# Kernel optimization log

Measured on AMD Instinct MI355X. Metric: run time of the kernel, lower is better.

Reference implementation:

```python
import jax, jax.numpy as jnp
import numpy as np
import math

B, S, D, H = 16, 1024, 1024, 16
HD = D // H                      # 64 head dim
MLP_H = int(int(D * 4.0) * 2 / 3)  # 2730 SwiGLU hidden
EPS = 1e-6


def _rmsnorm(h, w):
    # fp32 RMSNorm over last dim
    v = jnp.mean(h * h, axis=-1, keepdims=True)
    return w * (h * jax.lax.rsqrt(v + EPS))


def _rope(x):
    # x: [B, H, S, HD]; standard rotary, half-split convention
    hd = x.shape[-1]
    pos = jnp.arange(x.shape[-2], dtype=jnp.float32)
    inv = 1.0 / (10000.0 ** (jnp.arange(0, hd, 2, dtype=jnp.float32) / hd))
    fr = pos[:, None] * inv[None, :]          # [S, HD/2]
    cos, sin = jnp.cos(fr), jnp.sin(fr)
    x1, x2 = jnp.split(x, 2, axis=-1)
    return jnp.concatenate([x1 * cos - x2 * sin, x1 * sin + x2 * cos], axis=-1)


def setup_inputs() -> dict:
    key = jax.random.key(0)
    ks = jax.random.split(key, 16)
    sc = 0.02
    return {
        "x": jax.random.normal(ks[0], (B, S, D), jnp.float32),
        "c": jax.random.normal(ks[1], (B, D), jnp.float32),
        "w_qkv": jax.random.normal(ks[2], (D, 3 * D), jnp.float32) * sc,
        "b_qkv": jnp.zeros((3 * D,), jnp.float32),
        "w_proj": jax.random.normal(ks[3], (D, D), jnp.float32) * sc,
        "b_proj": jnp.zeros((D,), jnp.float32),
        "w12": jax.random.normal(ks[4], (D, 2 * MLP_H), jnp.float32) * sc,
        "b12": jnp.zeros((2 * MLP_H,), jnp.float32),
        "w3": jax.random.normal(ks[5], (MLP_H, D), jnp.float32) * sc,
        "b3": jnp.zeros((D,), jnp.float32),
        "w_ada": jax.random.normal(ks[6], (D, 6 * D), jnp.float32) * sc,
        "b_ada": jnp.zeros((6 * D,), jnp.float32),
        "norm1_w": jnp.ones((D,), jnp.float32),
        "norm2_w": jnp.ones((D,), jnp.float32),
        "qn_w": jnp.ones((HD,), jnp.float32),
        "kn_w": jnp.ones((HD,), jnp.float32),
    }


def _forward(x, c, w_qkv, b_qkv, w_proj, b_proj, w12, b12, w3, b3,
             w_ada, b_ada, norm1_w, norm2_w, qn_w, kn_w):
    # adaLN modulation params
    ada = jax.nn.silu(c) @ w_ada + b_ada               # [B, 6D]
    sh_a, sc_a, g_a, sh_m, sc_m, g_m = jnp.split(ada, 6, axis=-1)

    def modulate(h, shift, scale):
        return h * (1.0 + scale[:, None, :]) + shift[:, None, :]

    # --- attention branch ---
    h = modulate(_rmsnorm(x, norm1_w), sh_a, sc_a)     # [B, S, D]
    qkv = (h @ w_qkv + b_qkv).reshape(B, S, 3, H, HD)
    qkv = jnp.transpose(qkv, (2, 0, 3, 1, 4))          # [3, B, H, S, HD]
    q, k, v = qkv[0], qkv[1], qkv[2]
    q = _rope(_rmsnorm(q, qn_w))
    k = _rope(_rmsnorm(k, kn_w))
    scores = jnp.einsum('bhqd,bhkd->bhqk', q, k) / math.sqrt(HD)
    attn = jax.nn.softmax(scores, axis=-1)
    o = jnp.einsum('bhqk,bhkd->bhqd', attn, v)         # [B, H, S, HD]
    o = jnp.transpose(o, (0, 2, 1, 3)).reshape(B, S, D)
    o = o @ w_proj + b_proj
    x = x + g_a[:, None, :] * o

    # --- SwiGLU MLP branch ---
    h = modulate(_rmsnorm(x, norm2_w), sh_m, sc_m)
    x12 = h @ w12 + b12
    x1, x2 = jnp.split(x12, 2, axis=-1)
    mlp = (jax.nn.silu(x1) * x2) @ w3 + b3
    return x + g_m[:, None, :] * mlp


def reference(x, c, w_qkv, b_qkv, w_proj, b_proj, w12, b12, w3, b3,
              w_ada, b_ada, norm1_w, norm2_w, qn_w, kn_w):
    return _forward(x, c, w_qkv, b_qkv, w_proj, b_proj, w12, b12, w3, b3,
                    w_ada, b_ada, norm1_w, norm2_w, qn_w, kn_w)
```

## Files before the change

### kernel.cpp

```cpp
#include <hip/hip_runtime.h>
#include <hip/hip_bf16.h>
#include <math.h>

namespace {

constexpr int Bb = 16;
constexpr int Ss = 1024;
constexpr int Dd = 1024;
constexpr int Hh = 16;
constexpr int HD = 64;
constexpr int MLPH = 2730;
constexpr int MLPH_PAD = 2752;
constexpr int ADA_LD = 6144;
constexpr int NR = Bb * Ss;

typedef __attribute__((ext_vector_type(8))) short bf16x8;
typedef __attribute__((ext_vector_type(4))) float f32x4;
typedef __hip_bfloat16 bf16;
typedef unsigned int u32;

__device__ __forceinline__ float bf2f(bf16 v){ return __bfloat162float(v); }
__device__ __forceinline__ bf16 f2bf(float v){ return __float2bfloat16(v); }
__device__ __forceinline__ short f2bfs(float v){ bf16 t = __float2bfloat16(v); return __builtin_bit_cast(short, t); }

__device__ __forceinline__ f32x4 mfma16(bf16x8 a, bf16x8 b, f32x4 c){
  return __builtin_amdgcn_mfma_f32_16x16x32_bf16(a, b, c, 0, 0, 0);
}

__device__ __forceinline__ void gload16(const void* g, void* l){
  __builtin_amdgcn_global_load_lds(
      (const __attribute__((address_space(1))) u32*)g,
      (__attribute__((address_space(3))) u32*)l, 16, 0, 0);
}


__global__ void k_silu(const float* __restrict__ c, float* __restrict__ out, int n){
  int i = blockIdx.x*256 + threadIdx.x;
  if(i < n){ float v = c[i]; out[i] = v / (1.f + __expf(-v)); }
}

__global__ __launch_bounds__(256) void k_ada(const float* __restrict__ sc,
    const float* __restrict__ w, const float* __restrict__ bias, float* __restrict__ ada){
  __shared__ float red[4][Bb][64];
  int tid = threadIdx.x;
  int jj = tid & 63, ks = tid >> 6;
  int j = blockIdx.x*64 + jj;
  float acc[Bb];
  #pragma unroll
  for(int b=0;b<Bb;++b) acc[b] = 0.f;
  for(int k=ks*256; k<ks*256+256; ++k){
    float wv = w[(size_t)k*ADA_LD + j];
    #pragma unroll
    for(int b=0;b<Bb;++b) acc[b] += sc[b*Dd + k] * wv;
  }
  #pragma unroll
  for(int b=0;b<Bb;++b) red[ks][b][jj] = acc[b];
  __syncthreads();
  #pragma unroll
  for(int rep=0;rep<4;++rep){
    int idx = rep*256 + tid;
    int b = idx >> 6, j2 = idx & 63;
    float s = red[0][b][j2]+red[1][b][j2]+red[2][b][j2]+red[3][b][j2];
    ada[(size_t)b*ADA_LD + blockIdx.x*64 + j2] = s + bias[blockIdx.x*64 + j2];
  }
}

__global__ void k_rope_tab(float2* __restrict__ tab){
  int i = blockIdx.x*256 + threadIdx.x;
  int s = i >> 5, f = i & 31;
  float inv = powf(10000.f, -((float)(2*f)) / 64.f);
  float fr = (float)s * inv;
  float sv, cv;
  sincosf(fr, &sv, &cv);
  tab[i] = make_float2(cv, sv);
}

__global__ void k_transpose(const float* __restrict__ in, bf16* __restrict__ out,
                            int R, int C, int Rpad){
  __shared__ short tile[32][33];
  int tx = threadIdx.x & 31, ty = threadIdx.x >> 5;
  int tr0 = blockIdx.x*32, tc0 = blockIdx.y*32;
  #pragma unroll
  for(int i=0;i<4;++i){
    int r = tr0 + ty + i*8, cc = tc0 + tx;
    short v = 0;
    if(r < R && cc < C) v = f2bfs(in[(size_t)r*C + cc]);
    tile[ty+i*8][tx] = v;
  }
  __syncthreads();
  #pragma unroll
  for(int i=0;i<4;++i){
    int oc = tc0 + ty + i*8;
    int orow = tr0 + tx;
    if(oc < C && orow < Rpad)
      out[(size_t)oc*Rpad + orow] = __builtin_bit_cast(bf16, tile[tx][ty+i*8]);
  }
}

__global__ __launch_bounds__(256) void k_norm_mod(const float* __restrict__ x,
    const float* __restrict__ w, const float* __restrict__ shift, const float* __restrict__ scale,
    bf16* __restrict__ out){
  int r = blockIdx.x;
  int b = r >> 10;
  int t = threadIdx.x;
  const float* xr = x + (size_t)r*Dd;
  float v[4]; float ss = 0.f;
  #pragma unroll
  for(int i=0;i<4;++i){
    float f = xr[t*4+i];
    v[i] = f; ss += f*f;
  }
  #pragma unroll
  for(int m=1;m<64;m<<=1) ss += __shfl_xor(ss, m);
  __shared__ float red[4];
  if((t & 63) == 0) red[t>>6] = ss;
  __syncthreads();
  float tot = red[0]+red[1]+red[2]+red[3];
  float rms = rsqrtf(tot * (1.f/Dd) + 1e-6f);
  #pragma unroll
  for(int i=0;i<4;++i){
    int ccol = t*4+i;
    float h = v[i]*rms*w[ccol];
    float scv = scale[(size_t)b*ADA_LD + ccol];
    float shv = shift[(size_t)b*ADA_LD + ccol];
    out[(size_t)r*Dd + ccol] = f2bf(h*(1.f+scv) + shv);
  }
}

__global__ __launch_bounds__(256) void k_qknorm(bf16* __restrict__ qkv,
    const float* __restrict__ qw, const float* __restrict__ kw,
    const float2* __restrict__ tab){
  int bs = blockIdx.x;
  int s = bs & (Ss-1);
  int tid = threadIdx.x;
  int wv = tid >> 6, lane = tid & 63;
  int isK = wv >> 1;
  int chunk = (wv & 1)*64 + lane;
  int c = chunk & 7;
  int h = chunk >> 3;
  int dih = c*8;
  bf16* p = qkv + (size_t)bs*3072 + isK*Dd + h*HD + dih;
  bf16x8 v = *(const bf16x8*)p;
  float x[8]; float ss = 0.f;
  #pragma unroll
  for(int i=0;i<8;++i){ x[i] = bf2f(__builtin_bit_cast(bf16,(short)v[i])); ss += x[i]*x[i]; }
  ss += __shfl_xor(ss,1); ss += __shfl_xor(ss,2); ss += __shfl_xor(ss,4);
  float rms = rsqrtf(ss*(1.f/HD) + 1e-6f);
  const float* wn = isK ? kw : qw;
  float xn[8];
  #pragma unroll
  for(int i=0;i<8;++i) xn[i] = x[i]*rms*wn[dih+i];
  u32 pk[4], pq[4];
  #pragma unroll
  for(int i=0;i<4;++i)
    pk[i] = (u32)(unsigned short)f2bfs(xn[2*i]) |
            ((u32)(unsigned short)f2bfs(xn[2*i+1]) << 16);
  #pragma unroll
  for(int i=0;i<4;++i) pq[i] = __shfl_xor((int)pk[i], 4);
  float px[8];
  #pragma unroll
  for(int i=0;i<4;++i){
    px[2*i]   = bf2f(__builtin_bit_cast(bf16,(short)(pq[i] & 0xffff)));
    px[2*i+1] = bf2f(__builtin_bit_cast(bf16,(short)(pq[i] >> 16)));
  }
  const float2* tb = tab + s*32 + (c & 3)*8;
  float qs = isK ? 1.f : 0.18033688f;
  bf16x8 o;
  #pragma unroll
  for(int i=0;i<8;++i){
    float2 cs = tb[i];
    float r = (c < 4) ? (xn[i]*cs.x - px[i]*cs.y) : (px[i]*cs.y + xn[i]*cs.x);
    o[i] = f2bfs(r*qs);
  }
  *(bf16x8*)p = o;
}

#define LDA8(M,KH) (*(const bf16x8*)&Ah[((M)*16 + l15)*64 + ((((KH)*4 + l4) ^ l7))*8])
#define PHASE8(M0, STAGE_STMT, GATE_STMT) do{ \
  bf16x8 a0k0 = LDA8(M0,0), a0k1 = LDA8(M0,1), a1k0 = LDA8(M0+1,0), a1k1 = LDA8(M0+1,1); \
  STAGE_STMT; \
  __builtin_amdgcn_s_barrier(); \
  asm volatile("s_waitcnt lgkmcnt(0)" ::: "memory"); \
  __builtin_amdgcn_sched_barrier(0); \
  __builtin_amdgcn_s_setprio(1); \
  acc[M0][0]=mfma16(a0k0,bfrag[0][0],acc[M0][0]); acc[M0][0]=mfma16(a0k1,bfrag[0][1],acc[M0][0]); \
  acc[M0][1]=mfma16(a0k0,bfrag[1][0],acc[M0][1]); acc[M0][1]=mfma16(a0k1,bfrag[1][1],acc[M0][1]); \
  acc[M0][2]=mfma16(a0k0,bfrag[2][0],acc[M0][2]); acc[M0][2]=mfma16(a0k1,bfrag[2][1],acc[M0][2]); \
  acc[M0][3]=mfma16(a0k0,bfrag[3][0],acc[M0][3]); acc[M0][3]=mfma16(a0k1,bfrag[3][1],acc[M0][3]); \
  acc[M0+1][0]=mfma16(a1k0,bfrag[0][0],acc[M0+1][0]); acc[M0+1][0]=mfma16(a1k1,bfrag[0][1],acc[M0+1][0]); \
  acc[M0+1][1]=mfma16(a1k0,bfrag[1][0],acc[M0+1][1]); acc[M0+1][1]=mfma16(a1k1,bfrag[1][1],acc[M0+1][1]); \
  acc[M0+1][2]=mfma16(a1k0,bfrag[2][0],acc[M0+1][2]); acc[M0+1][2]=mfma16(a1k1,bfrag[2][1],acc[M0+1][2]); \
  acc[M0+1][3]=mfma16(a1k0,bfrag[3][0],acc[M0+1][3]); acc[M0+1][3]=mfma16(a1k1,bfrag[3][1],acc[M0+1][3]); \
  __builtin_amdgcn_s_setprio(0); \
  GATE_STMT; \
  __builtin_amdgcn_s_barrier(); }while(0)

template<int MODE>
__global__ __launch_bounds__(512, 2) void k_gemm8(
    const bf16* __restrict__ A, int lda,
    const bf16* __restrict__ BT, int ldb,
    const float* __restrict__ bias1, int K,
    const float* __restrict__ res, const float* __restrict__ gate,
    void* __restrict__ outp, int ldo)
{
  alignas(16) __shared__ short AH[2][2][128*64];
  alignas(16) __shared__ short BH[2][2][128*64];

  const int tid = threadIdx.x;
  const int lane = tid & 63, wid = tid >> 6;
  const int wm = wid >> 2, wn = wid & 3;
  const int l15 = lane & 15, l4 = lane >> 4;
  const int l7 = l15 & 7;
  const int brow = blockIdx.x * 256;
  const int bcol = blockIdx.y * 256;

  const int sr0 = tid >> 3;
  const int sr1 = sr0 + 64;
  const int sc  = ((tid & 7) ^ (sr0 & 7)) * 8;

  const bf16* Abase = A  + (size_t)brow*lda;
  const bf16* Bbase = BT + (size_t)bcol*ldb;

  auto stageA = [&](int t, int h){
    int d = t & 1;
    const bf16* g = Abase + (size_t)(h*128)*lda + t*64;
    gload16(g + (size_t)sr0*lda + sc, &AH[d][h][tid*8]);
    gload16(g + (size_t)sr1*lda + sc, &AH[d][h][(tid+512)*8]);
  };
  auto stageB = [&](int t, int h){
    int d = t & 1;
    const bf16* g = Bbase + (size_t)(h*128)*ldb + t*64;
    gload16(g + (size_t)sr0*ldb + sc, &BH[d][h][tid*8]);
    gload16(g + (size_t)sr1*ldb + sc, &BH[d][h][(tid+512)*8]);
  };

  f32x4 acc[8][4];
  f32x4 zero4 = {0.f,0.f,0.f,0.f};
  #pragma unroll
  for(int m=0;m<8;++m)
    #pragma unroll
    for(int n=0;n<4;++n) acc[m][n] = zero4;

  const int NT = K >> 6;
  stageA(0,0); stageA(0,1); stageB(0,0); stageB(0,1);
  stageB(1,0); stageB(1,1);
  asm volatile("s_waitcnt vmcnt(4)" ::: "memory");
  __builtin_amdgcn_sched_barrier(0);
  __builtin_amdgcn_s_barrier();

  const int bhsel = wn >> 1, brB = (wn & 1)*64;
  bf16x8 bfrag[4][2];

  for(int t=0; t<NT; ++t){
    const int d = t & 1;
    const short* Ah = AH[d][wm];
    const short* Bh = BH[d][bhsel];
    #pragma unroll
    for(int n=0;n<4;++n){
      int r = brB + n*16 + l15;
      bfrag[n][0] = *(const bf16x8*)&Bh[r*64 + ((l4     ^ l7))*8];
      bfrag[n][1] = *(const bf16x8*)&Bh[r*64 + (((4|l4) ^ l7))*8];
    }
    PHASE8(0, if(t+1 < NT) stageA(t+1,0), );
    PHASE8(2, if(t+1 < NT) stageA(t+1,1), );
    PHASE8(4, if(t+2 < NT) stageB(t+2,0), );
    PHASE8(6, if(t+2 < NT) stageB(t+2,1),
           asm volatile("s_waitcnt vmcnt(4)" ::: "memory");
           __builtin_amdgcn_sched_barrier(0) );
  }

  #pragma unroll
  for(int m=0;m<8;++m)
    #pragma unroll
    for(int n=0;n<4;++n)
      #pragma unroll
      for(int j=0;j<4;++j){
        int r  = brow + wm*128 + m*16 + l4*4 + j;
        int cc = bcol + wn*64  + n*16 + l15;
        float v = acc[m][n][j] + bias1[cc];
        if constexpr (MODE==0){
          ((bf16*)outp)[(size_t)r*ldo + cc] = f2bf(v);
        } else {
          int b = r >> 10;
          ((float*)outp)[(size_t)r*ldo + cc] =
              res[(size_t)r*Dd + cc] + gate[(size_t)b*ADA_LD + cc]*v;
        }
      }
}

__global__ __launch_bounds__(256, 2) void k_gemm3(
    const bf16* __restrict__ A, int lda,
    const bf16* __restrict__ BT, long long b2off, int ldb,
    const float* __restrict__ bias1, const float* __restrict__ bias2,
    int K, bf16* __restrict__ outp, int ldo)
{
  alignas(16) __shared__ short As[2][128*32];
  alignas(16) __shared__ short Bs[2][64*32];
  alignas(16) __shared__ short Bs2[2][64*32];

  int tid = threadIdx.x;
  int lane = tid & 63, wid = tid >> 6;
  int wm = wid >> 1, wn = wid & 1;
  int l15 = lane & 15, l4 = lane >> 4;
  int brow = blockIdx.x * 128;
  int bcol = blockIdx.y * 64;

  int r0 = tid >> 2, s0 = tid & 3;
  int r1 = r0 + 64;
  int k80 = s0 ^ ((r0 >> 1) & 3);
  int k81 = s0 ^ ((r1 >> 1) & 3);

  const bf16* a0 = A  + (size_t)(brow+r0)*lda + k80*8;
  const bf16* a1 = A  + (size_t)(brow+r1)*lda + k81*8;
  const bf16* b0 = BT + (size_t)(bcol+r0)*ldb + k80*8;

  f32x4 zero4 = {0.f,0.f,0.f,0.f};
  f32x4 acc[4][2], acc2[4][2];
  #pragma unroll
  for(int m=0;m<4;++m)
    #pragma unroll
    for(int n=0;n<2;++n){ acc[m][n]=zero4; acc2[m][n]=zero4; }

  auto STAGE = [&](int kt, int buf){
    int ko = kt << 5;
    gload16(a0 + ko, &As[buf][tid*8]);
    gload16(a1 + ko, &As[buf][(tid+256)*8]);
    gload16(b0 + ko, &Bs[buf][tid*8]);
    gload16(b0 + b2off + ko, &Bs2[buf][tid*8]);
  };

  const int nk = K >> 5;
  STAGE(0, 0);
  __syncthreads();

  int cur = 0;
  for(int kt=0; kt<nk; ++kt){
    if(kt+1 < nk) STAGE(kt+1, cur^1);
    bf16x8 af[4], bfr[2], bfr2[2];
    #pragma unroll
    for(int m=0;m<4;++m){
      int rr = wm*64 + m*16 + l15;
      int sl = l4 ^ ((rr >> 1) & 3);
      af[m] = *(const bf16x8*)&As[cur][rr*32 + sl*8];
    }
    #pragma unroll
    for(int n=0;n<2;++n){
      int rr = wn*32 + n*16 + l15;
      int sl = l4 ^ ((rr >> 1) & 3);
      bfr[n]  = *(const bf16x8*)&Bs[cur][rr*32 + sl*8];
      bfr2[n] = *(const bf16x8*)&Bs2[cur][rr*32 + sl*8];
    }
    #pragma unroll
    for(int m=0;m<4;++m)
      #pragma unroll
      for(int n=0;n<2;++n){
        acc[m][n]  = mfma16(af[m], bfr[n],  acc[m][n]);
        acc2[m][n] = mfma16(af[m], bfr2[n], acc2[m][n]);
      }
    __syncthreads();
    cur ^= 1;
  }

  #pragma unroll
  for(int m=0;m<4;++m)
    #pragma unroll
    for(int n=0;n<2;++n)
      #pragma unroll
      for(int j=0;j<4;++j){
        int r  = brow + wm*64 + m*16 + l4*4 + j;
        int cc = bcol + wn*32 + n*16 + l15;
        float o = 0.f;
        if(cc < MLPH){
          float v1 = acc[m][n][j] + bias1[cc];
          float v2 = acc2[m][n][j] + bias2[cc];
          o = (v1/(1.f+__expf(-v1)))*v2;
        }
        outp[(size_t)r*ldo + cc] = f2bf(o);
      }
}

__global__ __launch_bounds__(256) void k_attn(const bf16* __restrict__ qkv, bf16* __restrict__ obuf){
  alignas(16) __shared__ short Ks[64*64];
  alignas(16) __shared__ short VTs[64*64];
  alignas(16) __shared__ short Ps[128*64];

  int flatb = blockIdx.x;
  int low3 = flatb & 7;
  int rest = flatb >> 3;
  int qb   = rest & 7;
  int bh   = ((rest >> 3) << 3) | low3;
  int b = bh >> 4, h = bh & 15;

  int tid = threadIdx.x;
  int lane = tid & 63, w = tid >> 6;
  int l15 = lane & 15, l4 = lane >> 4;

  const bf16* base = qkv + (size_t)b*Ss*3072 + h*HD;

  bf16x8 aq[2][2];
  #pragma unroll
  for(int hi=0;hi<2;++hi)
    #pragma unroll
    for(int hf=0;hf<2;++hf)
      aq[hi][hf] = *(const bf16x8*)(base +
          (size_t)(qb*128 + w*32 + hi*16 + l15)*3072 + hf*32 + l4*8);

  int r0 = tid >> 3, c0 = tid & 7;
  int khcol = (c0 ^ (r0 & 7)) * 8;
  bf16x8 kreg[2], vreg[2];
  #pragma unroll
  for(int ch=0; ch<2; ++ch){
    int rr = r0 + ch*32;
    kreg[ch] = *(const bf16x8*)(base + Dd   + (size_t)rr*3072 + khcol);
    vreg[ch] = *(const bf16x8*)(base + 2*Dd + (size_t)rr*3072 + c0*8);
  }

  f32x4 zero4 = {0.f,0.f,0.f,0.f};
  f32x4 acc_o[2][4];
  float mrow[2], lrow[2];
  #pragma unroll
  for(int hi=0;hi<2;++hi){
    mrow[hi] = -1e30f; lrow[hi] = 0.f;
    #pragma unroll
    for(int an=0;an<4;++an) acc_o[hi][an] = zero4;
  }

  const float THR = 11.54f;

  for(int kb=0; kb<Ss/64; ++kb){
    if(kb) __syncthreads();
    #pragma unroll
    for(int ch=0; ch<2; ++ch){
      *(bf16x8*)&Ks[(tid + ch*256)*8] = kreg[ch];
      int vr = r0 + ch*32;
      #pragma unroll
      for(int i=0;i<8;++i){
        int g = i ^ c0;
        VTs[(c0*8 + i)*64 + (vr ^ (g<<3))] = vreg[ch][i];
      }
    }
    if(kb+1 < Ss/64){
      #pragma unroll
      for(int ch=0; ch<2; ++ch){
        int rr = (kb+1)*64 + r0 + ch*32;
        kreg[ch] = *(const bf16x8*)(base + Dd   + (size_t)rr*3072 + khcol);
        vreg[ch] = *(const bf16x8*)(base + 2*Dd + (size_t)rr*3072 + c0*8);
      }
    }
    __syncthreads();

    #pragma unroll
    for(int hi=0; hi<2; ++hi){
      f32x4 sacc[4];
      #pragma unroll
      for(int an=0;an<4;++an) sacc[an]=zero4;
      __builtin_amdgcn_s_setprio(1);
      #pragma unroll
      for(int an=0;an<4;++an){
        int R = an*16 + l15;
        bf16x8 bk0 = *(const bf16x8*)&Ks[R*64 + ((l4     ^ (R&7)))*8];
        bf16x8 bk1 = *(const bf16x8*)&Ks[R*64 + (((4|l4) ^ (R&7)))*8];
        sacc[an] = mfma16(bk0, aq[hi][0], sacc[an]);
        sacc[an] = mfma16(bk1, aq[hi][1], sacc[an]);
      }
      __builtin_amdgcn_s_setprio(0);

      float mx = -1e30f;
      #pragma unroll
      for(int an=0;an<4;++an)
        #pragma unroll
        for(int j=0;j<4;++j) mx = fmaxf(mx, sacc[an][j]);
      mx = fmaxf(mx, __shfl_xor(mx, 16));
      mx = fmaxf(mx, __shfl_xor(mx, 32));
      bool grow = mx > mrow[hi] + THR;
      if(__any(grow)){
        float mnew = fmaxf(mrow[hi], mx);
        float corr = exp2f(mrow[hi] - mnew);
        mrow[hi] = mnew;
        lrow[hi] *= corr;
        float cj[4];
        #pragma unroll
        for(int j=0;j<4;++j) cj[j] = __shfl(corr, l4*4 + j);
        #pragma unroll
        for(int an=0;an<4;++an)
          #pragma unroll
          for(int j=0;j<4;++j) acc_o[hi][an][j] *= cj[j];
      }
      float psum = 0.f;
      #pragma unroll
      for(int an=0;an<4;++an)
        #pragma unroll
        for(int j=0;j<4;++j){
          float pv = exp2f(sacc[an][j] - mrow[hi]);
          sacc[an][j] = pv; psum += pv;
        }
      psum += __shfl_xor(psum, 16);
      psum += __shfl_xor(psum, 32);
      lrow[hi] += psum;

      int prow = w*32 + hi*16 + l15;
      int pg = (l15 & 7) << 3;
      #pragma unroll
      for(int an=0;an<4;++an)
        #pragma unroll
        for(int j=0;j<4;++j)
          Ps[prow*64 + ((an*16 + l4*4 + j) ^ pg)] = f2bfs(sacc[an][j]);
      bf16x8 pa0 = *(const bf16x8*)&Ps[prow*64 + ((l4*8)      ^ pg)];
      bf16x8 pa1 = *(const bf16x8*)&Ps[prow*64 + ((32 + l4*8) ^ pg)];
      __builtin_amdgcn_s_setprio(1);
      #pragma unroll
      for(int an2=0;an2<4;++an2){
        int dR = an2*16 + l15;
        int g = ((dR & 7) ^ ((dR >> 3) & 7)) << 3;
        bf16x8 bv0 = *(const bf16x8*)&VTs[dR*64 + ((l4*8)      ^ g)];
        bf16x8 bv1 = *(const bf16x8*)&VTs[dR*64 + ((32 + l4*8) ^ g)];
        acc_o[hi][an2] = mfma16(pa0, bv0, acc_o[hi][an2]);
        acc_o[hi][an2] = mfma16(pa1, bv1, acc_o[hi][an2]);
      }
      __builtin_amdgcn_s_setprio(0);
    }
  }
  #pragma unroll
  for(int hi=0;hi<2;++hi){
    float lr[4];
    #pragma unroll
    for(int j=0;j<4;++j) lr[j] = __shfl(lrow[hi], l4*4 + j);
    #pragma unroll
    for(int an2=0;an2<4;++an2)
      #pragma unroll
      for(int j=0;j<4;++j){
        int r = qb*128 + w*32 + hi*16 + l4*4 + j;
        float ov = acc_o[hi][an2][j] / lr[j];
        obuf[((size_t)b*Ss + r)*Dd + h*HD + an2*16 + l15] = f2bf(ov);
      }
  }
}

}

extern "C" void kernel_launch(void* const* d_in, const int* in_sizes, int n_in,
                              void* d_out, int out_size, void* d_ws, size_t ws_size,
                              hipStream_t stream){
  const float* x      = (const float*)d_in[0];
  const float* c      = (const float*)d_in[1];
  const float* w_qkv  = (const float*)d_in[2];
  const float* b_qkv  = (const float*)d_in[3];
  const float* w_proj = (const float*)d_in[4];
  const float* b_proj = (const float*)d_in[5];
  const float* w12    = (const float*)d_in[6];
  const float* b12    = (const float*)d_in[7];
  const float* w3     = (const float*)d_in[8];
  const float* b3     = (const float*)d_in[9];
  const float* w_ada  = (const float*)d_in[10];
  const float* b_ada  = (const float*)d_in[11];
  const float* n1w    = (const float*)d_in[12];
  const float* n2w    = (const float*)d_in[13];
  const float* qnw    = (const float*)d_in[14];
  const float* knw    = (const float*)d_in[15];
  float* out = (float*)d_out;
  (void)in_sizes; (void)n_in; (void)out_size;

  constexpr size_t WS_NEED = 227254272ull;
  if (ws_size < WS_NEED) return;

  char* ws = (char*)d_ws;
  float*  silu_c = (float*)(ws + 0);
  float*  ada    = (float*)(ws + 65536);
  float2* ropet  = (float2*)(ws + 458752);
  bf16*   wqkvT  = (bf16*)(ws + 720896);
  bf16*   wprojT = (bf16*)(ws + 7012352);
  bf16*   w12T   = (bf16*)(ws + 9109504);
  bf16*   w3T    = (bf16*)(ws + 20291584);
  bf16*   hbuf   = (bf16*)(ws + 25927680);
  bf16*   qkvb   = (bf16*)(ws + 59482112);
  float*  xmid   = (float*)(ws + 160145408);
  bf16*   obuf   = hbuf;
  bf16*   h2     = hbuf;
  bf16*   mlpmid = qkvb;

  k_silu<<<64,256,0,stream>>>(c, silu_c, Bb*Dd);
  k_rope_tab<<<128,256,0,stream>>>(ropet);
  k_ada<<<96,256,0,stream>>>(silu_c, w_ada, b_ada, ada);
  k_transpose<<<dim3(32,96),256,0,stream>>>(w_qkv, wqkvT, 1024, 3072, 1024);
  k_transpose<<<dim3(32,32),256,0,stream>>>(w_proj, wprojT, 1024, 1024, 1024);
  k_transpose<<<dim3(32,171),256,0,stream>>>(w12, w12T, 1024, 5460, 1024);
  k_transpose<<<dim3(86,32),256,0,stream>>>(w3, w3T, 2730, 1024, 2752);

  k_norm_mod<<<NR,256,0,stream>>>(x, n1w, ada + 0, ada + 1024, hbuf);
  k_gemm8<0><<<dim3(64,12),512,0,stream>>>(hbuf,1024, wqkvT,1024,
      b_qkv, 1024, nullptr,nullptr, qkvb,3072);
  k_qknorm<<<NR,256,0,stream>>>(qkvb, qnw, knw, ropet);
  k_attn<<<2048,256,0,stream>>>(qkvb, obuf);
  k_gemm8<1><<<dim3(64,4),512,0,stream>>>(obuf,1024, wprojT,1024,
      b_proj, 1024, x, ada + 2048, xmid,1024);

  k_norm_mod<<<NR,256,0,stream>>>(xmid, n2w, ada + 3072, ada + 4096, h2);
  k_gemm3<<<dim3(128,43),256,0,stream>>>(h2,1024, w12T,(long long)MLPH*1024,1024,
      b12, b12 + MLPH, 1024, mlpmid, MLPH_PAD);
  k_gemm8<1><<<dim3(64,4),512,0,stream>>>(mlpmid,MLPH_PAD, w3T,MLPH_PAD,
      b3, MLPH_PAD, xmid, ada + 5120, out,1024);
}
```

Before: 891.5 us.

## Interleave W1/W2 columns and run SwiGLU GEMM through the big-tile gemm8 kernel

```diff
diff --git a/kernel.cpp b/kernel.cpp
--- a/kernel.cpp
+++ b/kernel.cpp
@@ -94,6 +94,31 @@
     int orow = tr0 + tx;
     if(oc < C && orow < Rpad)
       out[(size_t)oc*Rpad + orow] = __builtin_bit_cast(bf16, tile[tx][ty+i*8]);
+  }
+}
+
+__global__ void k_transpose12(const float* __restrict__ in, bf16* __restrict__ out){
+  __shared__ short tile[2][32][33];
+  int tx = threadIdx.x & 31, ty = threadIdx.x >> 5;
+  int tr0 = blockIdx.x*32, pc0 = blockIdx.y*32;
+  #pragma unroll
+  for(int i=0;i<4;++i){
+    int r = tr0 + ty + i*8, c = pc0 + tx;
+    short v1 = 0, v2 = 0;
+    if(c < MLPH){
+      v1 = f2bfs(in[(size_t)r*5460 + c]);
+      v2 = f2bfs(in[(size_t)r*5460 + MLPH + c]);
+    }
+    tile[0][ty+i*8][tx] = v1;
+    tile[1][ty+i*8][tx] = v2;
+  }
+  __syncthreads();
+  #pragma unroll
+  for(int i=0;i<4;++i){
+    int pc = pc0 + ty + i*8;
+    int orow = tr0 + tx;
+    out[(size_t)(2*pc  )*1024 + orow] = __builtin_bit_cast(bf16, tile[0][tx][ty+i*8]);
+    out[(size_t)(2*pc+1)*1024 + orow] = __builtin_bit_cast(bf16, tile[1][tx][ty+i*8]);
   }
 }
 
@@ -277,105 +302,26 @@
       for(int j=0;j<4;++j){
         int r  = brow + wm*128 + m*16 + l4*4 + j;
         int cc = bcol + wn*64  + n*16 + l15;
-        float v = acc[m][n][j] + bias1[cc];
         if constexpr (MODE==0){
+          float v = acc[m][n][j] + bias1[cc];
           ((bf16*)outp)[(size_t)r*ldo + cc] = f2bf(v);
-        } else {
+        } else if constexpr (MODE==1){
+          float v = acc[m][n][j] + bias1[cc];
           int b = r >> 10;
           ((float*)outp)[(size_t)r*ldo + cc] =
               res[(size_t)r*Dd + cc] + gate[(size_t)b*ADA_LD + cc]*v;
+        } else {
+          int pc = cc >> 1;
+          float bias = (pc < MLPH) ? bias1[(cc & 1) ? MLPH + pc : pc] : 0.f;
+          float v = acc[m][n][j] + bias;
+          float pv = __shfl_xor(v, 1);
+          if(!(l15 & 1)){
+            float o = 0.f;
+            if(pc < MLPH) o = (v/(1.f+__expf(-v)))*pv;
+            if(pc < MLPH_PAD)
+              ((bf16*)outp)[(size_t)r*ldo + pc] = f2bf(o);
+          }
         }
-      }
-}
-
-__global__ __launch_bounds__(256, 2) void k_gemm3(
-    const bf16* __restrict__ A, int lda,
-    const bf16* __restrict__ BT, long long b2off, int ldb,
-    const float* __restrict__ bias1, const float* __restrict__ bias2,
-    int K, bf16* __restrict__ outp, int ldo)
-{
-  alignas(16) __shared__ short As[2][128*32];
-  alignas(16) __shared__ short Bs[2][64*32];
-  alignas(16) __shared__ short Bs2[2][64*32];
-
-  int tid = threadIdx.x;
-  int lane = tid & 63, wid = tid >> 6;
-  int wm = wid >> 1, wn = wid & 1;
-  int l15 = lane & 15, l4 = lane >> 4;
-  int brow = blockIdx.x * 128;
-  int bcol = blockIdx.y * 64;
-
-  int r0 = tid >> 2, s0 = tid & 3;
-  int r1 = r0 + 64;
-  int k80 = s0 ^ ((r0 >> 1) & 3);
-  int k81 = s0 ^ ((r1 >> 1) & 3);
-
-  const bf16* a0 = A  + (size_t)(brow+r0)*lda + k80*8;
-  const bf16* a1 = A  + (size_t)(brow+r1)*lda + k81*8;
-  const bf16* b0 = BT + (size_t)(bcol+r0)*ldb + k80*8;
-
-  f32x4 zero4 = {0.f,0.f,0.f,0.f};
-  f32x4 acc[4][2], acc2[4][2];
-  #pragma unroll
-  for(int m=0;m<4;++m)
-    #pragma unroll
-    for(int n=0;n<2;++n){ acc[m][n]=zero4; acc2[m][n]=zero4; }
-
-  auto STAGE = [&](int kt, int buf){
-    int ko = kt << 5;
-    gload16(a0 + ko, &As[buf][tid*8]);
-    gload16(a1 + ko, &As[buf][(tid+256)*8]);
-    gload16(b0 + ko, &Bs[buf][tid*8]);
-    gload16(b0 + b2off + ko, &Bs2[buf][tid*8]);
-  };
-
-  const int nk = K >> 5;
-  STAGE(0, 0);
-  __syncthreads();
-
-  int cur = 0;
-  for(int kt=0; kt<nk; ++kt){
-    if(kt+1 < nk) STAGE(kt+1, cur^1);
-    bf16x8 af[4], bfr[2], bfr2[2];
-    #pragma unroll
-    for(int m=0;m<4;++m){
-      int rr = wm*64 + m*16 + l15;
-      int sl = l4 ^ ((rr >> 1) & 3);
-      af[m] = *(const bf16x8*)&As[cur][rr*32 + sl*8];
-    }
-    #pragma unroll
-    for(int n=0;n<2;++n){
-      int rr = wn*32 + n*16 + l15;
-      int sl = l4 ^ ((rr >> 1) & 3);
-      bfr[n]  = *(const bf16x8*)&Bs[cur][rr*32 + sl*8];
-      bfr2[n] = *(const bf16x8*)&Bs2[cur][rr*32 + sl*8];
-    }
-    #pragma unroll
-    for(int m=0;m<4;++m)
-      #pragma unroll
-      for(int n=0;n<2;++n){
-        acc[m][n]  = mfma16(af[m], bfr[n],  acc[m][n]);
-        acc2[m][n] = mfma16(af[m], bfr2[n], acc2[m][n]);
-      }
-    __syncthreads();
-    cur ^= 1;
-  }
-
-  #pragma unroll
-  for(int m=0;m<4;++m)
-    #pragma unroll
-    for(int n=0;n<2;++n)
-      #pragma unroll
-      for(int j=0;j<4;++j){
-        int r  = brow + wm*64 + m*16 + l4*4 + j;
-        int cc = bcol + wn*32 + n*16 + l15;
-        float o = 0.f;
-        if(cc < MLPH){
-          float v1 = acc[m][n][j] + bias1[cc];
-          float v2 = acc2[m][n][j] + bias2[cc];
-          o = (v1/(1.f+__expf(-v1)))*v2;
-        }
-        outp[(size_t)r*ldo + cc] = f2bf(o);
       }
 }
 
@@ -569,7 +515,7 @@
   float2* ropet  = (float2*)(ws + 458752);
   bf16*   wqkvT  = (bf16*)(ws + 720896);
   bf16*   wprojT = (bf16*)(ws + 7012352);
-  bf16*   w12T   = (bf16*)(ws + 9109504);
+  bf16*   w12iT  = (bf16*)(ws + 720896);
   bf16*   w3T    = (bf16*)(ws + 20291584);
   bf16*   hbuf   = (bf16*)(ws + 25927680);
   bf16*   qkvb   = (bf16*)(ws + 59482112);
@@ -583,7 +529,6 @@
   k_ada<<<96,256,0,stream>>>(silu_c, w_ada, b_ada, ada);
   k_transpose<<<dim3(32,96),256,0,stream>>>(w_qkv, wqkvT, 1024, 3072, 1024);
   k_transpose<<<dim3(32,32),256,0,stream>>>(w_proj, wprojT, 1024, 1024, 1024);
-  k_transpose<<<dim3(32,171),256,0,stream>>>(w12, w12T, 1024, 5460, 1024);
   k_transpose<<<dim3(86,32),256,0,stream>>>(w3, w3T, 2730, 1024, 2752);
 
   k_norm_mod<<<NR,256,0,stream>>>(x, n1w, ada + 0, ada + 1024, hbuf);
@@ -594,9 +539,10 @@
   k_gemm8<1><<<dim3(64,4),512,0,stream>>>(obuf,1024, wprojT,1024,
       b_proj, 1024, x, ada + 2048, xmid,1024);
 
+  k_transpose12<<<dim3(32,88),256,0,stream>>>(w12, w12iT);
   k_norm_mod<<<NR,256,0,stream>>>(xmid, n2w, ada + 3072, ada + 4096, h2);
-  k_gemm3<<<dim3(128,43),256,0,stream>>>(h2,1024, w12T,(long long)MLPH*1024,1024,
-      b12, b12 + MLPH, 1024, mlpmid, MLPH_PAD);
+  k_gemm8<2><<<dim3(64,22),512,0,stream>>>(h2,1024, w12iT,1024,
+      b12, 1024, nullptr,nullptr, mlpmid, MLPH_PAD);
   k_gemm8<1><<<dim3(64,4),512,0,stream>>>(mlpmid,MLPH_PAD, w3T,MLPH_PAD,
       b3, MLPH_PAD, xmid, ada + 5120, out,1024);
 }
```

Measured after the change: 989.0 us. 1.11x slower.
